# Kernel tuning notes

Measured on AMD Instinct MI355X. Metric: run time of the kernel, lower is better.

## Reference

```python
import jax, jax.numpy as jnp
import numpy as np

N_NODES = 50000
N_EDGES = 600000
DIM = 128
N_LAYERS = 3
N_GRAPHS = 512
BN_EPS = 1e-5


def setup_inputs() -> dict:
    key = jax.random.key(0)
    ks = jax.random.split(key, 8)
    x = jax.random.normal(ks[0], (N_NODES, DIM), dtype=jnp.float32)
    edge_index = jax.random.randint(ks[1], (2, N_EDGES), 0, N_NODES, dtype=jnp.int32)
    batch = jnp.sort(jax.random.randint(ks[2], (N_NODES,), 0, N_GRAPHS, dtype=jnp.int32))
    W1s = jax.random.normal(ks[3], (N_LAYERS, DIM, DIM), dtype=jnp.float32) * (1.0 / np.sqrt(DIM))
    b1s = jnp.zeros((N_LAYERS, DIM), dtype=jnp.float32)
    W2s = jax.random.normal(ks[4], (N_LAYERS, DIM, DIM), dtype=jnp.float32) * (1.0 / np.sqrt(DIM))
    b2s = jnp.zeros((N_LAYERS, DIM), dtype=jnp.float32)
    gammas = jnp.ones((N_LAYERS, DIM), dtype=jnp.float32)
    betas = jnp.zeros((N_LAYERS, DIM), dtype=jnp.float32)
    return {"x": x, "edge_index": edge_index, "batch": batch,
            "W1s": W1s, "b1s": b1s, "W2s": W2s, "b2s": b2s,
            "gammas": gammas, "betas": betas}


def reference(x, edge_index, batch, W1s, b1s, W2s, b2s, gammas, betas):
    # EncoderGIN.forward: stack of GINConv (eps=0) -> ReLU -> BatchNorm1d (train mode),
    # then global_add_pool per layer and concat along feature dim.
    n_nodes = x.shape[0]
    src, dst = edge_index[0], edge_index[1]
    h = x
    pools = []
    for i in range(N_LAYERS):
        # GINConv: aggregate sum of neighbor feats at dst, add (1+0)*self
        agg = jax.ops.segment_sum(h[src], dst, num_segments=n_nodes) + h
        # MLP: Linear -> ReLU -> Linear
        h1 = jax.nn.relu(agg @ W1s[i] + b1s[i])
        h2 = h1 @ W2s[i] + b2s[i]
        # outer ReLU
        h2 = jax.nn.relu(h2)
        # BatchNorm1d, training mode (biased variance over the node dim)
        mean = jnp.mean(h2, axis=0)
        var = jnp.var(h2, axis=0)
        h = (h2 - mean) * jax.lax.rsqrt(var + BN_EPS) * gammas[i] + betas[i]
        pools.append(jax.ops.segment_sum(h, batch, num_segments=N_GRAPHS))
    return jnp.concatenate(pools, axis=1)  # [N_GRAPHS, N_LAYERS*DIM]
```

## Files before the change

### kernel.cpp

```cpp
#include <hip/hip_runtime.h>

#define N_NODES 50000
#define N_EDGES 600000
#define DIM 128
#define N_GRAPHS 512
#define N_LAYERS 3
#define OUT_STRIDE (N_LAYERS * DIM)
#define BN_EPS 1e-5f
#define N_REP 16
#define CAP 64

#define NPB 128
#define NBIN 391
#define BCAP_BIN 3072
#define PADC 16
#define EPB 4096
#define NB3 147

typedef __attribute__((ext_vector_type(8))) short short8;
typedef __attribute__((ext_vector_type(4))) float floatx4;

__device__ inline short f2bf(float f) {
    union { float f; unsigned u; } x{f};
    unsigned r = x.u + 0x7fffu + ((x.u >> 16) & 1u);
    return (short)(r >> 16);
}
__device__ inline float bf2f(short h) {
    union { unsigned u; float f; } x;
    x.u = ((unsigned)(unsigned short)h) << 16;
    return x.f;
}
__device__ inline void split_trunc(float f, short& hi, short& lo) {
    union { float f; unsigned u; } x{f};
    hi = (short)(x.u >> 16);
    union { unsigned u; float f; } hf;
    hf.u = x.u & 0xffff0000u;
    union { float f; unsigned u; } y{f - hf.f};
    lo = (short)(y.u >> 16);
}
__device__ inline floatx4 bf4_to_f4(uint2 w) {
    union { unsigned u; float f; } a, b, c, d;
    a.u = w.x << 16;
    b.u = w.x & 0xffff0000u;
    c.u = w.y << 16;
    d.u = w.y & 0xffff0000u;
    return floatx4{a.f, b.f, c.f, d.f};
}

__global__ __launch_bounds__(256) void prep_scatter_kernel(const int* __restrict__ src,
                                                           const int* __restrict__ dst,
                                                           int* __restrict__ binCur,
                                                           int2* __restrict__ binned,
                                                           const float* __restrict__ W1s,
                                                           const float* __restrict__ W2s,
                                                           short* __restrict__ Whi,
                                                           short* __restrict__ Wlo,
                                                           const float* __restrict__ x,
                                                           short* __restrict__ xb,
                                                           short* __restrict__ hbA,
                                                           short* __restrict__ hbB) {
    if (blockIdx.x < NB3) {
        __shared__ int hist[NBIN];
        __shared__ int basev[NBIN];
        const int t = threadIdx.x;
        for (int b = t; b < NBIN; b += 256) hist[b] = 0;
        __syncthreads();
        const int e0 = blockIdx.x * EPB;
        int sreg[16], dreg[16], rreg[16];
#pragma unroll
        for (int k = 0; k < 16; ++k) {
            int e = e0 + k * 256 + t;
            if (e < N_EDGES) {
                sreg[k] = src[e];
                dreg[k] = dst[e];
            } else {
                dreg[k] = -1;
            }
        }
#pragma unroll
        for (int k = 0; k < 16; ++k)
            if (dreg[k] >= 0) rreg[k] = atomicAdd(&hist[dreg[k] >> 7], 1);
        __syncthreads();
        for (int b = t; b < NBIN; b += 256) {
            int c = hist[b];
            basev[b] = (c > 0) ? atomicAdd(&binCur[b * PADC], c) : 0;
        }
        __syncthreads();
#pragma unroll
        for (int k = 0; k < 16; ++k)
            if (dreg[k] >= 0) {
                int b = dreg[k] >> 7;
                int pos = basev[b] + rreg[k];
                if (pos < BCAP_BIN)
                    binned[(size_t)b * BCAP_BIN + pos] = make_int2(sreg[k], dreg[k] & (NPB - 1));
            }
        return;
    }
    int i = (blockIdx.x - NB3) * 256 + threadIdx.x;
    if (i < 6 * DIM * DIM) {
        int mat = i >> 14;
        int e = i & 16383;
        int k = e >> 7, n = e & 127;
        const float* W = (mat < 3) ? (W1s + (size_t)mat * DIM * DIM)
                                   : (W2s + (size_t)(mat - 3) * DIM * DIM);
        float w = W[e];
        short hi = f2bf(w);
        short lo = f2bf(w - bf2f(hi));
        size_t o = ((size_t)mat << 14) + n * DIM + k;
        Whi[o] = hi;
        Wlo[o] = lo;
    }
    if (i < N_NODES * 32) {
        float4 v = ((const float4*)x)[i];
        unsigned lo = (unsigned short)f2bf(v.x) | ((unsigned)(unsigned short)f2bf(v.y) << 16);
        unsigned hi = (unsigned short)f2bf(v.z) | ((unsigned)(unsigned short)f2bf(v.w) << 16);
        ((uint2*)xb)[i] = make_uint2(lo, hi);
    } else if (i < (N_NODES + 1) * 32) {
        ((uint2*)xb)[i] = make_uint2(0u, 0u);
        ((uint2*)hbA)[i] = make_uint2(0u, 0u);
        ((uint2*)hbB)[i] = make_uint2(0u, 0u);
    }
}

__global__ __launch_bounds__(256) void bucket_build_kernel(const int* __restrict__ binCur,
                                                           const int2* __restrict__ binned,
                                                           int* __restrict__ deg,
                                                           int* __restrict__ esrc) {
    __shared__ int ldeg[NPB];
    __shared__ int lbuck[NPB * CAP];
    const int b = blockIdx.x;
    const int t = threadIdx.x;
    for (int i = t; i < NPB * CAP; i += 256) lbuck[i] = N_NODES;
    if (t < NPB) ldeg[t] = 0;
    __syncthreads();
    int n = binCur[b * PADC];
    if (n > BCAP_BIN) n = BCAP_BIN;
    const int2* bp = binned + (size_t)b * BCAP_BIN;
    for (int i = t; i < n; i += 256) {
        int2 e = bp[i];
        int slot = atomicAdd(&ldeg[e.y], 1);
        if (slot < CAP) lbuck[(e.y << 6) + slot] = e.x;
    }
    __syncthreads();
    const int node0 = b * NPB;
    const int nvalid = min(NPB, N_NODES - node0);
    if (t < NPB && t < nvalid) deg[node0 + t] = ldeg[t];
    const int nu4 = nvalid << 4;
    uint4* d4 = (uint4*)(esrc + ((size_t)node0 << 6));
    const uint4* s4 = (const uint4*)lbuck;
    for (int i = t; i < nu4; i += 256) d4[i] = s4[i];
}

__global__ __launch_bounds__(256, 4) void fused_layer_kernel(
    const short* __restrict__ hin,
    const int* __restrict__ deg,
    const int* __restrict__ esrc,
    const float* __restrict__ prevrep,
    const float* __restrict__ pgamma,
    const float* __restrict__ pbeta,
    const short* __restrict__ W1hi, const short* __restrict__ W1lo,
    const float* __restrict__ b1,
    const short* __restrict__ W2hi, const short* __restrict__ W2lo,
    const float* __restrict__ b2,
    const int* __restrict__ batch,
    short* __restrict__ out,
    float* __restrict__ srep,
    float* __restrict__ gout,
    int layer) {
    __shared__ unsigned sbuf[4096];
    __shared__ float GO_s[256];
    short* As_hi = (short*)sbuf;
    short* As_lo = (short*)(sbuf + 2048);
    const int tid = threadIdx.x;
    const int base = blockIdx.x * 32;

    const int hw = tid >> 5;
    const int l32 = tid & 31;
    int dgr_r[4];
    uint4 idx_r[4][4];
#pragma unroll
    for (int i = 0; i < 4; ++i) {
        int node = base + hw * 4 + i;
        int nc = (node < N_NODES) ? node : (N_NODES - 1);
        dgr_r[i] = deg[nc];
        const uint4* ep = (const uint4*)(esrc + ((size_t)nc << 6));
#pragma unroll
        for (int q = 0; q < 4; ++q) idx_r[i][q] = ep[q];
    }

    if (prevrep) {
        float s = 0.f;
#pragma unroll
        for (int r = 0; r < N_REP; ++r) s += prevrep[r * 256 + tid];
        GO_s[tid] = s;
        __syncthreads();
        if (tid < 128) {
            const float invn = 1.0f / (float)N_NODES;
            float m = GO_s[tid] * invn;
            float var = GO_s[128 + tid] * invn - m * m;
            float G = pgamma[tid] * rsqrtf(var + BN_EPS);
            GO_s[tid] = G;
            GO_s[128 + tid] = pbeta[tid] - m * G;
        }
    } else {
        GO_s[tid] = (tid < 128) ? 1.f : 0.f;
    }
    __syncthreads();

    {
        floatx4 G4 = *(const floatx4*)&GO_s[4 * l32];
        floatx4 O4 = *(const floatx4*)&GO_s[128 + 4 * l32];
        const uint2* hb = (const uint2*)hin;
#pragma unroll
        for (int i = 0; i < 4; ++i) {
            int r = hw * 4 + i;
            int node = base + r;
            floatx4 acc = {0.f, 0.f, 0.f, 0.f};
            if (node < N_NODES) {
                int dgr = dgr_r[i];
                if (dgr > CAP) dgr = CAP;
                uint2 wv[16];
                uint2 wself = hb[(size_t)node * 32 + l32];
#pragma unroll
                for (int q = 0; q < 4; ++q) {
                    uint4 iq = idx_r[i][q];
                    wv[4 * q + 0] = hb[(size_t)iq.x * 32 + l32];
                    wv[4 * q + 1] = hb[(size_t)iq.y * 32 + l32];
                    wv[4 * q + 2] = hb[(size_t)iq.z * 32 + l32];
                    wv[4 * q + 3] = hb[(size_t)iq.w * 32 + l32];
                }
                floatx4 t0 = (bf4_to_f4(wv[0]) + bf4_to_f4(wv[1])) + (bf4_to_f4(wv[2]) + bf4_to_f4(wv[3]));
                floatx4 t1 = (bf4_to_f4(wv[4]) + bf4_to_f4(wv[5])) + (bf4_to_f4(wv[6]) + bf4_to_f4(wv[7]));
                floatx4 t2 = (bf4_to_f4(wv[8]) + bf4_to_f4(wv[9])) + (bf4_to_f4(wv[10]) + bf4_to_f4(wv[11]));
                floatx4 t3 = (bf4_to_f4(wv[12]) + bf4_to_f4(wv[13])) + (bf4_to_f4(wv[14]) + bf4_to_f4(wv[15]));
                acc = bf4_to_f4(wself) + ((t0 + t1) + (t2 + t3));
                if (dgr > 16) {
                    int b0 = node << 6;
                    int jend = b0 + ((dgr + 7) & ~7);
                    for (int j = b0 + 16; j < jend; j += 8) {
                        uint4 i0 = *(const uint4*)&esrc[j];
                        uint4 i1 = *(const uint4*)&esrc[j + 4];
                        uint2 w0 = hb[(size_t)i0.x * 32 + l32];
                        uint2 w1 = hb[(size_t)i0.y * 32 + l32];
                        uint2 w2 = hb[(size_t)i0.z * 32 + l32];
                        uint2 w3 = hb[(size_t)i0.w * 32 + l32];
                        uint2 w4 = hb[(size_t)i1.x * 32 + l32];
                        uint2 w5 = hb[(size_t)i1.y * 32 + l32];
                        uint2 w6 = hb[(size_t)i1.z * 32 + l32];
                        uint2 w7 = hb[(size_t)i1.w * 32 + l32];
                        acc += ((bf4_to_f4(w0) + bf4_to_f4(w1)) + (bf4_to_f4(w2) + bf4_to_f4(w3))) +
                               ((bf4_to_f4(w4) + bf4_to_f4(w5)) + (bf4_to_f4(w6) + bf4_to_f4(w7)));
                    }
                }
                float dp1 = (float)(dgr + 1);
                acc = G4 * acc + dp1 * O4;
            }
            short hi[4], lo[4];
#pragma unroll
            for (int q = 0; q < 4; ++q) split_trunc(acc[q], hi[q], lo[q]);
            unsigned h0 = (unsigned short)hi[0] | ((unsigned)(unsigned short)hi[1] << 16);
            unsigned h1 = (unsigned short)hi[2] | ((unsigned)(unsigned short)hi[3] << 16);
            unsigned l0 = (unsigned short)lo[0] | ((unsigned)(unsigned short)lo[1] << 16);
            unsigned l1 = (unsigned short)lo[2] | ((unsigned)(unsigned short)lo[3] << 16);
            int ch = l32 >> 1, half = l32 & 1;
            int pos = r * 128 + ((ch ^ (r & 15)) * 8) + half * 4;
            *(uint2*)&As_hi[pos] = make_uint2(h0, h1);
            *(uint2*)&As_lo[pos] = make_uint2(l0, l1);
        }
    }
    __syncthreads();

    const int wave = tid >> 6;
    const int lane = tid & 63;
    const int l15 = lane & 15;
    const int quad = lane >> 4;

    floatx4 acc[2][2];
#pragma unroll
    for (int mi = 0; mi < 2; ++mi)
#pragma unroll
        for (int nl = 0; nl < 2; ++nl) acc[mi][nl] = floatx4{0.f, 0.f, 0.f, 0.f};
#pragma unroll
    for (int ks = 0; ks < 4; ++ks) {
        short8 ahi[2], alo[2], bhi[2], blo[2];
#pragma unroll
        for (int mi = 0; mi < 2; ++mi) {
            int row = mi * 16 + l15;
            int pos = row * 128 + (((ks * 4 + quad) ^ l15) * 8);
            ahi[mi] = *(const short8*)&As_hi[pos];
            alo[mi] = *(const short8*)&As_lo[pos];
        }
#pragma unroll
        for (int nl = 0; nl < 2; ++nl) {
            size_t p = (size_t)((wave * 2 + nl) * 16 + l15) * DIM + ks * 32 + quad * 8;
            bhi[nl] = *(const short8*)&W1hi[p];
            blo[nl] = *(const short8*)&W1lo[p];
        }
#pragma unroll
        for (int mi = 0; mi < 2; ++mi)
#pragma unroll
            for (int nl = 0; nl < 2; ++nl) {
                acc[mi][nl] = __builtin_amdgcn_mfma_f32_16x16x32_bf16(ahi[mi], bhi[nl], acc[mi][nl], 0, 0, 0);
                acc[mi][nl] = __builtin_amdgcn_mfma_f32_16x16x32_bf16(alo[mi], bhi[nl], acc[mi][nl], 0, 0, 0);
                acc[mi][nl] = __builtin_amdgcn_mfma_f32_16x16x32_bf16(ahi[mi], blo[nl], acc[mi][nl], 0, 0, 0);
            }
    }
    __syncthreads();

#pragma unroll
    for (int mi = 0; mi < 2; ++mi)
#pragma unroll
        for (int nl = 0; nl < 2; ++nl) {
            int col = (wave * 2 + nl) * 16 + l15;
            float bv = b1[col];
#pragma unroll
            for (int reg = 0; reg < 4; ++reg) {
                int row = mi * 16 + quad * 4 + reg;
                float v = fmaxf(acc[mi][nl][reg] + bv, 0.f);
                union { float f; unsigned u; } x{v};
                union { unsigned u; float f; } hf;
                hf.u = x.u & 0xffff0000u;
                union { float f; unsigned u; } y{v - hf.f};
                unsigned w = hf.u | (y.u >> 16);
                sbuf[row * 128 + ((((col >> 2) ^ (row & 31)) * 4) + (col & 3))] = w;
            }
        }
    __syncthreads();

    floatx4 acc2[2][2];
#pragma unroll
    for (int mi = 0; mi < 2; ++mi)
#pragma unroll
        for (int nl = 0; nl < 2; ++nl) acc2[mi][nl] = floatx4{0.f, 0.f, 0.f, 0.f};
#pragma unroll
    for (int ks = 0; ks < 4; ++ks) {
        short8 ahi2[2], alo2[2], bhi[2], blo[2];
#pragma unroll
        for (int mi = 0; mi < 2; ++mi) {
            int row = mi * 16 + l15;
            int c5 = ks * 8 + quad * 2;
            unsigned w[8];
            *(uint4*)&w[0] = *(const uint4*)&sbuf[row * 128 + ((c5 ^ (row & 31)) * 4)];
            *(uint4*)&w[4] = *(const uint4*)&sbuf[row * 128 + (((c5 + 1) ^ (row & 31)) * 4)];
#pragma unroll
            for (int j = 0; j < 8; ++j) {
                ahi2[mi][j] = (short)(w[j] >> 16);
                alo2[mi][j] = (short)(w[j] & 0xffffu);
            }
        }
#pragma unroll
        for (int nl = 0; nl < 2; ++nl) {
            size_t p = (size_t)((wave * 2 + nl) * 16 + l15) * DIM + ks * 32 + quad * 8;
            bhi[nl] = *(const short8*)&W2hi[p];
            blo[nl] = *(const short8*)&W2lo[p];
        }
#pragma unroll
        for (int mi = 0; mi < 2; ++mi)
#pragma unroll
            for (int nl = 0; nl < 2; ++nl) {
                acc2[mi][nl] = __builtin_amdgcn_mfma_f32_16x16x32_bf16(ahi2[mi], bhi[nl], acc2[mi][nl], 0, 0, 0);
                acc2[mi][nl] = __builtin_amdgcn_mfma_f32_16x16x32_bf16(alo2[mi], bhi[nl], acc2[mi][nl], 0, 0, 0);
                acc2[mi][nl] = __builtin_amdgcn_mfma_f32_16x16x32_bf16(ahi2[mi], blo[nl], acc2[mi][nl], 0, 0, 0);
            }
    }
    __syncthreads();

    float* pool_s = (float*)sbuf;
    float* ssum = (float*)sbuf + 384;
    float* ssq = (float*)sbuf + 512;

    const int g0 = batch[base];
    int idxr[2][4];
#pragma unroll
    for (int mi = 0; mi < 2; ++mi)
#pragma unroll
        for (int reg = 0; reg < 4; ++reg) {
            int row = base + mi * 16 + quad * 4 + reg;
            idxr[mi][reg] = (row < N_NODES) ? (batch[row] - g0) : -1;
        }

#pragma unroll
    for (int nl = 0; nl < 2; ++nl) {
        int col = (wave * 2 + nl) * 16 + l15;
        float bv = b2[col];
        float s_p = 0.f, q_p = 0.f, p0 = 0.f, p1 = 0.f, p2 = 0.f;
#pragma unroll
        for (int mi = 0; mi < 2; ++mi)
#pragma unroll
            for (int reg = 0; reg < 4; ++reg) {
                int idx = idxr[mi][reg];
                if (idx >= 0) {
                    int row = base + mi * 16 + quad * 4 + reg;
                    float v = fmaxf(acc2[mi][nl][reg] + bv, 0.f);
                    out[(size_t)row * DIM + col] = f2bf(v);
                    s_p += v;
                    q_p += v * v;
                    if (idx == 0) p0 += v;
                    else if (idx == 1) p1 += v;
                    else if (idx == 2) p2 += v;
                    else atomicAdd(&gout[(size_t)(g0 + idx) * OUT_STRIDE + layer * DIM + col], v);
                }
            }
        s_p += __shfl_xor(s_p, 16);
        s_p += __shfl_xor(s_p, 32);
        q_p += __shfl_xor(q_p, 16);
        q_p += __shfl_xor(q_p, 32);
        p0 += __shfl_xor(p0, 16);
        p0 += __shfl_xor(p0, 32);
        p1 += __shfl_xor(p1, 16);
        p1 += __shfl_xor(p1, 32);
        p2 += __shfl_xor(p2, 16);
        p2 += __shfl_xor(p2, 32);
        if (quad == 0) {
            ssum[col] = s_p;
            ssq[col] = q_p;
            pool_s[col] = p0;
            pool_s[128 + col] = p1;
            pool_s[256 + col] = p2;
        }
    }
    __syncthreads();

    float* srep_b = srep + (blockIdx.x & (N_REP - 1)) * 256;
    if (tid < 128)
        atomicAdd(&srep_b[tid], ssum[tid]);
    else
        atomicAdd(&srep_b[tid], ssq[tid - 128]);
    for (int i = tid; i < 384; i += 256) {
        int slot = i >> 7, col = i & 127;
        float pv = pool_s[slot * 128 + col];
        int g = g0 + slot;
        if (pv != 0.f && g < N_GRAPHS)
            atomicAdd(&gout[(size_t)g * OUT_STRIDE + layer * DIM + col], pv);
    }
}

__global__ __launch_bounds__(384) void finalize_kernel(const float* __restrict__ rep,
                                                       const float* __restrict__ gammas,
                                                       const float* __restrict__ betas,
                                                       const int* __restrict__ batch,
                                                       float* __restrict__ out) {
    __shared__ float cntf;
    int b = blockIdx.x;
    int t = threadIdx.x;
    if (t == 0) {
        int lo = 0, hi = N_NODES;
        while (lo < hi) {
            int m = (lo + hi) >> 1;
            if (batch[m] < b) lo = m + 1;
            else hi = m;
        }
        int lo2 = lo, hi2 = N_NODES;
        while (lo2 < hi2) {
            int m = (lo2 + hi2) >> 1;
            if (batch[m] < b + 1) lo2 = m + 1;
            else hi2 = m;
        }
        cntf = (float)(lo2 - lo);
    }
    __syncthreads();
    int l = t >> 7, c = t & 127;
    const float* rl = rep + (size_t)l * N_REP * 256;
    float s = 0.f, q = 0.f;
#pragma unroll
    for (int r = 0; r < N_REP; ++r) {
        s += rl[r * 256 + c];
        q += rl[r * 256 + 128 + c];
    }
    const float invn = 1.0f / (float)N_NODES;
    float m = s * invn;
    float var = q * invn - m * m;
    float G = gammas[l * DIM + c] * rsqrtf(var + BN_EPS);
    float OFF = betas[l * DIM + c] - m * G;
    size_t o = (size_t)b * OUT_STRIDE + t;
    out[o] = fmaf(G, out[o], cntf * OFF);
}

extern "C" void kernel_launch(void* const* d_in, const int* in_sizes, int n_in,
                              void* d_out, int out_size, void* d_ws, size_t ws_size,
                              hipStream_t stream) {
    const float* x = (const float*)d_in[0];
    const int* ei = (const int*)d_in[1];
    const int* srcp = ei;
    const int* dstp = ei + N_EDGES;
    const int* batch = (const int*)d_in[2];
    const float* W1s = (const float*)d_in[3];
    const float* b1s = (const float*)d_in[4];
    const float* W2s = (const float*)d_in[5];
    const float* b2s = (const float*)d_in[6];
    const float* gammas = (const float*)d_in[7];
    const float* betas = (const float*)d_in[8];
    float* out = (float*)d_out;

    const size_t NFR = (size_t)(N_NODES + 1) * DIM;
    short* hbufA = (short*)d_ws;
    short* hbufB = hbufA + NFR;
    short* xb = hbufB + NFR;
    short* whi = xb + NFR;
    short* wlo = whi + 6 * DIM * DIM;
    float* stats_rep = (float*)(wlo + 6 * DIM * DIM);
    int* binCur = (int*)(stats_rep + 3 * N_REP * 256);
    int* deg = binCur + NBIN * PADC;
    int* esrc = deg + N_NODES;
    int2* binned = (int2*)hbufB;

    hipMemsetAsync(out, 0, (size_t)N_GRAPHS * OUT_STRIDE * sizeof(float), stream);
    hipMemsetAsync(stats_rep, 0,
                   (3 * N_REP * 256) * sizeof(float) + (NBIN * PADC) * sizeof(int), stream);

    prep_scatter_kernel<<<NB3 + ((N_NODES + 1) * 32 + 255) / 256, 256, 0, stream>>>(
        srcp, dstp, binCur, binned, W1s, W2s, whi, wlo, x, xb, hbufA, hbufB);
    bucket_build_kernel<<<NBIN, 256, 0, stream>>>(binCur, binned, deg, esrc);

    const int nblk = (N_NODES + 31) / 32;
    const short* hin = xb;
    short* hout = hbufA;
    for (int layer = 0; layer < N_LAYERS; ++layer) {
        const float* prevrep =
            (layer == 0) ? nullptr : (stats_rep + (size_t)(layer - 1) * N_REP * 256);
        fused_layer_kernel<<<nblk, 256, 0, stream>>>(
            hin, deg, esrc, prevrep, gammas + (layer - 1) * DIM, betas + (layer - 1) * DIM,
            whi + ((size_t)layer << 14), wlo + ((size_t)layer << 14), b1s + layer * DIM,
            whi + ((size_t)(3 + layer) << 14), wlo + ((size_t)(3 + layer) << 14),
            b2s + layer * DIM, batch, hout, stats_rep + (size_t)layer * N_REP * 256, out, layer);
        hin = hout;
        hout = (hout == hbufA) ? hbufB : hbufA;
    }
    finalize_kernel<<<N_GRAPHS, 384, 0, stream>>>(stats_rep, gammas, betas, batch, out);
}
```

Measured before the change: 285.2 us.

## Process two node tiles per block and batch neighbor gathers in pairs

The fused layer kernel now loops over two 32-node tiles per block, halving the grid to 782 blocks. The per-block BN-coefficient prologue (summing 16 stat replicas) is amortized over both tiles. Neighbor gathers are issued two nodes at a time behind sched barriers to raise memory-level parallelism, and launch bounds drop to 3 waves per SIMD to give room for the extra registers. The risks are lower occupancy and fewer blocks to spread across the CUs, which can leave some idle and add tail imbalance.

```diff
diff --git a/kernel.cpp b/kernel.cpp
--- a/kernel.cpp
+++ b/kernel.cpp
@@ -16,6 +16,10 @@
 #define PADC 16
 #define EPB 4096
 #define NB3 147
+
+#define NTILES 1563
+#define TPB 2
+#define NBLK 782
 
 typedef __attribute__((ext_vector_type(8))) short short8;
 typedef __attribute__((ext_vector_type(4))) float floatx4;
@@ -151,7 +155,7 @@
     for (int i = t; i < nu4; i += 256) d4[i] = s4[i];
 }
 
-__global__ __launch_bounds__(256, 4) void fused_layer_kernel(
+__global__ __launch_bounds__(256, 3) void fused_layer_kernel(
     const short* __restrict__ hin,
     const int* __restrict__ deg,
     const int* __restrict__ esrc,
@@ -172,21 +176,12 @@
     short* As_hi = (short*)sbuf;
     short* As_lo = (short*)(sbuf + 2048);
     const int tid = threadIdx.x;
-    const int base = blockIdx.x * 32;
-
     const int hw = tid >> 5;
     const int l32 = tid & 31;
-    int dgr_r[4];
-    uint4 idx_r[4][4];
-#pragma unroll
-    for (int i = 0; i < 4; ++i) {
-        int node = base + hw * 4 + i;
-        int nc = (node < N_NODES) ? node : (N_NODES - 1);
-        dgr_r[i] = deg[nc];
-        const uint4* ep = (const uint4*)(esrc + ((size_t)nc << 6));
-#pragma unroll
-        for (int q = 0; q < 4; ++q) idx_r[i][q] = ep[q];
-    }
+    const int wave = tid >> 6;
+    const int lane = tid & 63;
+    const int l15 = lane & 15;
+    const int quad = lane >> 4;
 
     if (prevrep) {
         float s = 0.f;
@@ -207,231 +202,264 @@
     }
     __syncthreads();
 
-    {
-        floatx4 G4 = *(const floatx4*)&GO_s[4 * l32];
-        floatx4 O4 = *(const floatx4*)&GO_s[128 + 4 * l32];
-        const uint2* hb = (const uint2*)hin;
-#pragma unroll
-        for (int i = 0; i < 4; ++i) {
-            int r = hw * 4 + i;
-            int node = base + r;
-            floatx4 acc = {0.f, 0.f, 0.f, 0.f};
-            if (node < N_NODES) {
-                int dgr = dgr_r[i];
-                if (dgr > CAP) dgr = CAP;
-                uint2 wv[16];
-                uint2 wself = hb[(size_t)node * 32 + l32];
-#pragma unroll
-                for (int q = 0; q < 4; ++q) {
-                    uint4 iq = idx_r[i][q];
-                    wv[4 * q + 0] = hb[(size_t)iq.x * 32 + l32];
-                    wv[4 * q + 1] = hb[(size_t)iq.y * 32 + l32];
-                    wv[4 * q + 2] = hb[(size_t)iq.z * 32 + l32];
-                    wv[4 * q + 3] = hb[(size_t)iq.w * 32 + l32];
-                }
-                floatx4 t0 = (bf4_to_f4(wv[0]) + bf4_to_f4(wv[1])) + (bf4_to_f4(wv[2]) + bf4_to_f4(wv[3]));
-                floatx4 t1 = (bf4_to_f4(wv[4]) + bf4_to_f4(wv[5])) + (bf4_to_f4(wv[6]) + bf4_to_f4(wv[7]));
-                floatx4 t2 = (bf4_to_f4(wv[8]) + bf4_to_f4(wv[9])) + (bf4_to_f4(wv[10]) + bf4_to_f4(wv[11]));
-                floatx4 t3 = (bf4_to_f4(wv[12]) + bf4_to_f4(wv[13])) + (bf4_to_f4(wv[14]) + bf4_to_f4(wv[15]));
-                acc = bf4_to_f4(wself) + ((t0 + t1) + (t2 + t3));
-                if (dgr > 16) {
-                    int b0 = node << 6;
-                    int jend = b0 + ((dgr + 7) & ~7);
-                    for (int j = b0 + 16; j < jend; j += 8) {
-                        uint4 i0 = *(const uint4*)&esrc[j];
-                        uint4 i1 = *(const uint4*)&esrc[j + 4];
-                        uint2 w0 = hb[(size_t)i0.x * 32 + l32];
-                        uint2 w1 = hb[(size_t)i0.y * 32 + l32];
-                        uint2 w2 = hb[(size_t)i0.z * 32 + l32];
-                        uint2 w3 = hb[(size_t)i0.w * 32 + l32];
-                        uint2 w4 = hb[(size_t)i1.x * 32 + l32];
-                        uint2 w5 = hb[(size_t)i1.y * 32 + l32];
-                        uint2 w6 = hb[(size_t)i1.z * 32 + l32];
-                        uint2 w7 = hb[(size_t)i1.w * 32 + l32];
-                        acc += ((bf4_to_f4(w0) + bf4_to_f4(w1)) + (bf4_to_f4(w2) + bf4_to_f4(w3))) +
-                               ((bf4_to_f4(w4) + bf4_to_f4(w5)) + (bf4_to_f4(w6) + bf4_to_f4(w7)));
+    const uint2* hb = (const uint2*)hin;
+    floatx4 G4 = *(const floatx4*)&GO_s[4 * l32];
+    floatx4 O4 = *(const floatx4*)&GO_s[128 + 4 * l32];
+
+    for (int tk = 0; tk < TPB; ++tk) {
+        const int tile = blockIdx.x * TPB + tk;
+        if (tile >= NTILES) break;
+        const int base = tile * 32;
+
+        {
+            int dgr_r[4];
+            uint4 idx_r[4][4];
+#pragma unroll
+            for (int i = 0; i < 4; ++i) {
+                int node = base + hw * 4 + i;
+                int nc = (node < N_NODES) ? node : (N_NODES - 1);
+                dgr_r[i] = deg[nc];
+                const uint4* ep = (const uint4*)(esrc + ((size_t)nc << 6));
+#pragma unroll
+                for (int q = 0; q < 4; ++q) idx_r[i][q] = ep[q];
+            }
+            __builtin_amdgcn_sched_barrier(0);
+
+#pragma unroll
+            for (int pr = 0; pr < 2; ++pr) {
+                uint2 wself[2];
+                uint2 wv[2][16];
+#pragma unroll
+                for (int ii = 0; ii < 2; ++ii) {
+                    int i = pr * 2 + ii;
+                    int node = base + hw * 4 + i;
+                    int nc = (node < N_NODES) ? node : (N_NODES - 1);
+                    wself[ii] = hb[(size_t)nc * 32 + l32];
+#pragma unroll
+                    for (int q = 0; q < 4; ++q) {
+                        uint4 iq = idx_r[i][q];
+                        wv[ii][4 * q + 0] = hb[(size_t)iq.x * 32 + l32];
+                        wv[ii][4 * q + 1] = hb[(size_t)iq.y * 32 + l32];
+                        wv[ii][4 * q + 2] = hb[(size_t)iq.z * 32 + l32];
+                        wv[ii][4 * q + 3] = hb[(size_t)iq.w * 32 + l32];
                     }
                 }
-                float dp1 = (float)(dgr + 1);
-                acc = G4 * acc + dp1 * O4;
-            }
-            short hi[4], lo[4];
-#pragma unroll
-            for (int q = 0; q < 4; ++q) split_trunc(acc[q], hi[q], lo[q]);
-            unsigned h0 = (unsigned short)hi[0] | ((unsigned)(unsigned short)hi[1] << 16);
-            unsigned h1 = (unsigned short)hi[2] | ((unsigned)(unsigned short)hi[3] << 16);
-            unsigned l0 = (unsigned short)lo[0] | ((unsigned)(unsigned short)lo[1] << 16);
-            unsigned l1 = (unsigned short)lo[2] | ((unsigned)(unsigned short)lo[3] << 16);
-            int ch = l32 >> 1, half = l32 & 1;
-            int pos = r * 128 + ((ch ^ (r & 15)) * 8) + half * 4;
-            *(uint2*)&As_hi[pos] = make_uint2(h0, h1);
-            *(uint2*)&As_lo[pos] = make_uint2(l0, l1);
-        }
-    }
-    __syncthreads();
-
-    const int wave = tid >> 6;
-    const int lane = tid & 63;
-    const int l15 = lane & 15;
-    const int quad = lane >> 4;
-
-    floatx4 acc[2][2];
-#pragma unroll
-    for (int mi = 0; mi < 2; ++mi)
-#pragma unroll
-        for (int nl = 0; nl < 2; ++nl) acc[mi][nl] = floatx4{0.f, 0.f, 0.f, 0.f};
-#pragma unroll
-    for (int ks = 0; ks < 4; ++ks) {
-        short8 ahi[2], alo[2], bhi[2], blo[2];
-#pragma unroll
-        for (int mi = 0; mi < 2; ++mi) {
-            int row = mi * 16 + l15;
-            int pos = row * 128 + (((ks * 4 + quad) ^ l15) * 8);
-            ahi[mi] = *(const short8*)&As_hi[pos];
-            alo[mi] = *(const short8*)&As_lo[pos];
-        }
-#pragma unroll
-        for (int nl = 0; nl < 2; ++nl) {
-            size_t p = (size_t)((wave * 2 + nl) * 16 + l15) * DIM + ks * 32 + quad * 8;
-            bhi[nl] = *(const short8*)&W1hi[p];
-            blo[nl] = *(const short8*)&W1lo[p];
-        }
+                __builtin_amdgcn_sched_barrier(0);
+
+#pragma unroll
+                for (int ii = 0; ii < 2; ++ii) {
+                    int i = pr * 2 + ii;
+                    int r = hw * 4 + i;
+                    int node = base + r;
+                    floatx4 acc = {0.f, 0.f, 0.f, 0.f};
+                    if (node < N_NODES) {
+                        int dgr = dgr_r[i];
+                        if (dgr > CAP) dgr = CAP;
+                        floatx4 t0 = (bf4_to_f4(wv[ii][0]) + bf4_to_f4(wv[ii][1])) +
+                                     (bf4_to_f4(wv[ii][2]) + bf4_to_f4(wv[ii][3]));
+                        floatx4 t1 = (bf4_to_f4(wv[ii][4]) + bf4_to_f4(wv[ii][5])) +
+                                     (bf4_to_f4(wv[ii][6]) + bf4_to_f4(wv[ii][7]));
+                        floatx4 t2 = (bf4_to_f4(wv[ii][8]) + bf4_to_f4(wv[ii][9])) +
+                                     (bf4_to_f4(wv[ii][10]) + bf4_to_f4(wv[ii][11]));
+                        floatx4 t3 = (bf4_to_f4(wv[ii][12]) + bf4_to_f4(wv[ii][13])) +
+                                     (bf4_to_f4(wv[ii][14]) + bf4_to_f4(wv[ii][15]));
+                        acc = bf4_to_f4(wself[ii]) + ((t0 + t1) + (t2 + t3));
+                        if (dgr > 16) {
+                            int b0 = node << 6;
+                            int jend = b0 + ((dgr + 7) & ~7);
+                            for (int j = b0 + 16; j < jend; j += 8) {
+                                uint4 i0 = *(const uint4*)&esrc[j];
+                                uint4 i1 = *(const uint4*)&esrc[j + 4];
+                                uint2 w0 = hb[(size_t)i0.x * 32 + l32];
+                                uint2 w1 = hb[(size_t)i0.y * 32 + l32];
+                                uint2 w2 = hb[(size_t)i0.z * 32 + l32];
+                                uint2 w3 = hb[(size_t)i0.w * 32 + l32];
+                                uint2 w4 = hb[(size_t)i1.x * 32 + l32];
+                                uint2 w5 = hb[(size_t)i1.y * 32 + l32];
+                                uint2 w6 = hb[(size_t)i1.z * 32 + l32];
+                                uint2 w7 = hb[(size_t)i1.w * 32 + l32];
+                                acc += ((bf4_to_f4(w0) + bf4_to_f4(w1)) + (bf4_to_f4(w2) + bf4_to_f4(w3))) +
+                                       ((bf4_to_f4(w4) + bf4_to_f4(w5)) + (bf4_to_f4(w6) + bf4_to_f4(w7)));
+                            }
+                        }
+                        float dp1 = (float)(dgr + 1);
+                        acc = G4 * acc + dp1 * O4;
+                    }
+                    short hi[4], lo[4];
+#pragma unroll
+                    for (int q = 0; q < 4; ++q) split_trunc(acc[q], hi[q], lo[q]);
+                    unsigned h0 = (unsigned short)hi[0] | ((unsigned)(unsigned short)hi[1] << 16);
+                    unsigned h1 = (unsigned short)hi[2] | ((unsigned)(unsigned short)hi[3] << 16);
+                    unsigned l0 = (unsigned short)lo[0] | ((unsigned)(unsigned short)lo[1] << 16);
+                    unsigned l1 = (unsigned short)lo[2] | ((unsigned)(unsigned short)lo[3] << 16);
+                    int ch = l32 >> 1, half = l32 & 1;
+                    int pos = r * 128 + ((ch ^ (r & 15)) * 8) + half * 4;
+                    *(uint2*)&As_hi[pos] = make_uint2(h0, h1);
+                    *(uint2*)&As_lo[pos] = make_uint2(l0, l1);
+                }
+            }
+        }
+        __syncthreads();
+
+        floatx4 acc[2][2];
 #pragma unroll
         for (int mi = 0; mi < 2; ++mi)
 #pragma unroll
+            for (int nl = 0; nl < 2; ++nl) acc[mi][nl] = floatx4{0.f, 0.f, 0.f, 0.f};
+#pragma unroll
+        for (int ks = 0; ks < 4; ++ks) {
+            short8 ahi[2], alo[2], bhi[2], blo[2];
+#pragma unroll
+            for (int mi = 0; mi < 2; ++mi) {
+                int row = mi * 16 + l15;
+                int pos = row * 128 + (((ks * 4 + quad) ^ l15) * 8);
+                ahi[mi] = *(const short8*)&As_hi[pos];
+                alo[mi] = *(const short8*)&As_lo[pos];
+            }
+#pragma unroll
             for (int nl = 0; nl < 2; ++nl) {
-                acc[mi][nl] = __builtin_amdgcn_mfma_f32_16x16x32_bf16(ahi[mi], bhi[nl], acc[mi][nl], 0, 0, 0);
-                acc[mi][nl] = __builtin_amdgcn_mfma_f32_16x16x32_bf16(alo[mi], bhi[nl], acc[mi][nl], 0, 0, 0);
-                acc[mi][nl] = __builtin_amdgcn_mfma_f32_16x16x32_bf16(ahi[mi], blo[nl], acc[mi][nl], 0, 0, 0);
-            }
-    }
-    __syncthreads();
-
-#pragma unroll
-    for (int mi = 0; mi < 2; ++mi)
+                size_t p = (size_t)((wave * 2 + nl) * 16 + l15) * DIM + ks * 32 + quad * 8;
+                bhi[nl] = *(const short8*)&W1hi[p];
+                blo[nl] = *(const short8*)&W1lo[p];
+            }
+#pragma unroll
+            for (int mi = 0; mi < 2; ++mi)
+#pragma unroll
+                for (int nl = 0; nl < 2; ++nl) {
+                    acc[mi][nl] = __builtin_amdgcn_mfma_f32_16x16x32_bf16(ahi[mi], bhi[nl], acc[mi][nl], 0, 0, 0);
+                    acc[mi][nl] = __builtin_amdgcn_mfma_f32_16x16x32_bf16(alo[mi], bhi[nl], acc[mi][nl], 0, 0, 0);
+                    acc[mi][nl] = __builtin_amdgcn_mfma_f32_16x16x32_bf16(ahi[mi], blo[nl], acc[mi][nl], 0, 0, 0);
+                }
+        }
+        __syncthreads();
+
+#pragma unroll
+        for (int mi = 0; mi < 2; ++mi)
+#pragma unroll
+            for (int nl = 0; nl < 2; ++nl) {
+                int col = (wave * 2 + nl) * 16 + l15;
+                float bv = b1[col];
+#pragma unroll
+                for (int reg = 0; reg < 4; ++reg) {
+                    int row = mi * 16 + quad * 4 + reg;
+                    float v = fmaxf(acc[mi][nl][reg] + bv, 0.f);
+                    union { float f; unsigned u; } x{v};
+                    union { unsigned u; float f; } hf;
+                    hf.u = x.u & 0xffff0000u;
+                    union { float f; unsigned u; } y{v - hf.f};
+                    unsigned w = hf.u | (y.u >> 16);
+                    sbuf[row * 128 + ((((col >> 2) ^ (row & 31)) * 4) + (col & 3))] = w;
+                }
+            }
+        __syncthreads();
+
+        floatx4 acc2[2][2];
+#pragma unroll
+        for (int mi = 0; mi < 2; ++mi)
+#pragma unroll
+            for (int nl = 0; nl < 2; ++nl) acc2[mi][nl] = floatx4{0.f, 0.f, 0.f, 0.f};
+#pragma unroll
+        for (int ks = 0; ks < 4; ++ks) {
+            short8 ahi2[2], alo2[2], bhi[2], blo[2];
+#pragma unroll
+            for (int mi = 0; mi < 2; ++mi) {
+                int row = mi * 16 + l15;
+                int c5 = ks * 8 + quad * 2;
+                unsigned w[8];
+                *(uint4*)&w[0] = *(const uint4*)&sbuf[row * 128 + ((c5 ^ (row & 31)) * 4)];
+                *(uint4*)&w[4] = *(const uint4*)&sbuf[row * 128 + (((c5 + 1) ^ (row & 31)) * 4)];
+#pragma unroll
+                for (int j = 0; j < 8; ++j) {
+                    ahi2[mi][j] = (short)(w[j] >> 16);
+                    alo2[mi][j] = (short)(w[j] & 0xffffu);
+                }
+            }
+#pragma unroll
+            for (int nl = 0; nl < 2; ++nl) {
+                size_t p = (size_t)((wave * 2 + nl) * 16 + l15) * DIM + ks * 32 + quad * 8;
+                bhi[nl] = *(const short8*)&W2hi[p];
+                blo[nl] = *(const short8*)&W2lo[p];
+            }
+#pragma unroll
+            for (int mi = 0; mi < 2; ++mi)
+#pragma unroll
+                for (int nl = 0; nl < 2; ++nl) {
+                    acc2[mi][nl] = __builtin_amdgcn_mfma_f32_16x16x32_bf16(ahi2[mi], bhi[nl], acc2[mi][nl], 0, 0, 0);
+                    acc2[mi][nl] = __builtin_amdgcn_mfma_f32_16x16x32_bf16(alo2[mi], bhi[nl], acc2[mi][nl], 0, 0, 0);
+                    acc2[mi][nl] = __builtin_amdgcn_mfma_f32_16x16x32_bf16(ahi2[mi], blo[nl], acc2[mi][nl], 0, 0, 0);
+                }
+        }
+        __syncthreads();
+
+        float* pool_s = (float*)sbuf;
+        float* ssum = (float*)sbuf + 384;
+        float* ssq = (float*)sbuf + 512;
+
+        const int g0 = batch[base];
+        int idxr[2][4];
+#pragma unroll
+        for (int mi = 0; mi < 2; ++mi)
+#pragma unroll
+            for (int reg = 0; reg < 4; ++reg) {
+                int row = base + mi * 16 + quad * 4 + reg;
+                idxr[mi][reg] = (row < N_NODES) ? (batch[row] - g0) : -1;
+            }
+
 #pragma unroll
         for (int nl = 0; nl < 2; ++nl) {
             int col = (wave * 2 + nl) * 16 + l15;
-            float bv = b1[col];
-#pragma unroll
-            for (int reg = 0; reg < 4; ++reg) {
-                int row = mi * 16 + quad * 4 + reg;
-                float v = fmaxf(acc[mi][nl][reg] + bv, 0.f);
-                union { float f; unsigned u; } x{v};
-                union { unsigned u; float f; } hf;
-                hf.u = x.u & 0xffff0000u;
-                union { float f; unsigned u; } y{v - hf.f};
-                unsigned w = hf.u | (y.u >> 16);
-                sbuf[row * 128 + ((((col >> 2) ^ (row & 31)) * 4) + (col & 3))] = w;
-            }
-        }
-    __syncthreads();
-
-    floatx4 acc2[2][2];
-#pragma unroll
-    for (int mi = 0; mi < 2; ++mi)
-#pragma unroll
-        for (int nl = 0; nl < 2; ++nl) acc2[mi][nl] = floatx4{0.f, 0.f, 0.f, 0.f};
-#pragma unroll
-    for (int ks = 0; ks < 4; ++ks) {
-        short8 ahi2[2], alo2[2], bhi[2], blo[2];
-#pragma unroll
-        for (int mi = 0; mi < 2; ++mi) {
-            int row = mi * 16 + l15;
-            int c5 = ks * 8 + quad * 2;
-            unsigned w[8];
-            *(uint4*)&w[0] = *(const uint4*)&sbuf[row * 128 + ((c5 ^ (row & 31)) * 4)];
-            *(uint4*)&w[4] = *(const uint4*)&sbuf[row * 128 + (((c5 + 1) ^ (row & 31)) * 4)];
-#pragma unroll
-            for (int j = 0; j < 8; ++j) {
-                ahi2[mi][j] = (short)(w[j] >> 16);
-                alo2[mi][j] = (short)(w[j] & 0xffffu);
-            }
-        }
-#pragma unroll
-        for (int nl = 0; nl < 2; ++nl) {
-            size_t p = (size_t)((wave * 2 + nl) * 16 + l15) * DIM + ks * 32 + quad * 8;
-            bhi[nl] = *(const short8*)&W2hi[p];
-            blo[nl] = *(const short8*)&W2lo[p];
-        }
-#pragma unroll
-        for (int mi = 0; mi < 2; ++mi)
-#pragma unroll
-            for (int nl = 0; nl < 2; ++nl) {
-                acc2[mi][nl] = __builtin_amdgcn_mfma_f32_16x16x32_bf16(ahi2[mi], bhi[nl], acc2[mi][nl], 0, 0, 0);
-                acc2[mi][nl] = __builtin_amdgcn_mfma_f32_16x16x32_bf16(alo2[mi], bhi[nl], acc2[mi][nl], 0, 0, 0);
-                acc2[mi][nl] = __builtin_amdgcn_mfma_f32_16x16x32_bf16(ahi2[mi], blo[nl], acc2[mi][nl], 0, 0, 0);
-            }
-    }
-    __syncthreads();
-
-    float* pool_s = (float*)sbuf;
-    float* ssum = (float*)sbuf + 384;
-    float* ssq = (float*)sbuf + 512;
-
-    const int g0 = batch[base];
-    int idxr[2][4];
-#pragma unroll
-    for (int mi = 0; mi < 2; ++mi)
-#pragma unroll
-        for (int reg = 0; reg < 4; ++reg) {
-            int row = base + mi * 16 + quad * 4 + reg;
-            idxr[mi][reg] = (row < N_NODES) ? (batch[row] - g0) : -1;
-        }
-
-#pragma unroll
-    for (int nl = 0; nl < 2; ++nl) {
-        int col = (wave * 2 + nl) * 16 + l15;
-        float bv = b2[col];
-        float s_p = 0.f, q_p = 0.f, p0 = 0.f, p1 = 0.f, p2 = 0.f;
-#pragma unroll
-        for (int mi = 0; mi < 2; ++mi)
-#pragma unroll
-            for (int reg = 0; reg < 4; ++reg) {
-                int idx = idxr[mi][reg];
-                if (idx >= 0) {
-                    int row = base + mi * 16 + quad * 4 + reg;
-                    float v = fmaxf(acc2[mi][nl][reg] + bv, 0.f);
-                    out[(size_t)row * DIM + col] = f2bf(v);
-                    s_p += v;
-                    q_p += v * v;
-                    if (idx == 0) p0 += v;
-                    else if (idx == 1) p1 += v;
-                    else if (idx == 2) p2 += v;
-                    else atomicAdd(&gout[(size_t)(g0 + idx) * OUT_STRIDE + layer * DIM + col], v);
-                }
-            }
-        s_p += __shfl_xor(s_p, 16);
-        s_p += __shfl_xor(s_p, 32);
-        q_p += __shfl_xor(q_p, 16);
-        q_p += __shfl_xor(q_p, 32);
-        p0 += __shfl_xor(p0, 16);
-        p0 += __shfl_xor(p0, 32);
-        p1 += __shfl_xor(p1, 16);
-        p1 += __shfl_xor(p1, 32);
-        p2 += __shfl_xor(p2, 16);
-        p2 += __shfl_xor(p2, 32);
-        if (quad == 0) {
-            ssum[col] = s_p;
-            ssq[col] = q_p;
-            pool_s[col] = p0;
-            pool_s[128 + col] = p1;
-            pool_s[256 + col] = p2;
-        }
-    }
-    __syncthreads();
-
-    float* srep_b = srep + (blockIdx.x & (N_REP - 1)) * 256;
-    if (tid < 128)
-        atomicAdd(&srep_b[tid], ssum[tid]);
-    else
-        atomicAdd(&srep_b[tid], ssq[tid - 128]);
-    for (int i = tid; i < 384; i += 256) {
-        int slot = i >> 7, col = i & 127;
-        float pv = pool_s[slot * 128 + col];
-        int g = g0 + slot;
-        if (pv != 0.f && g < N_GRAPHS)
-            atomicAdd(&gout[(size_t)g * OUT_STRIDE + layer * DIM + col], pv);
+            float bv = b2[col];
+            float s_p = 0.f, q_p = 0.f, p0 = 0.f, p1 = 0.f, p2 = 0.f;
+#pragma unroll
+            for (int mi = 0; mi < 2; ++mi)
+#pragma unroll
+                for (int reg = 0; reg < 4; ++reg) {
+                    int idx = idxr[mi][reg];
+                    if (idx >= 0) {
+                        int row = base + mi * 16 + quad * 4 + reg;
+                        float v = fmaxf(acc2[mi][nl][reg] + bv, 0.f);
+                        out[(size_t)row * DIM + col] = f2bf(v);
+                        s_p += v;
+                        q_p += v * v;
+                        if (idx == 0) p0 += v;
+                        else if (idx == 1) p1 += v;
+                        else if (idx == 2) p2 += v;
+                        else atomicAdd(&gout[(size_t)(g0 + idx) * OUT_STRIDE + layer * DIM + col], v);
+                    }
+                }
+            s_p += __shfl_xor(s_p, 16);
+            s_p += __shfl_xor(s_p, 32);
+            q_p += __shfl_xor(q_p, 16);
+            q_p += __shfl_xor(q_p, 32);
+            p0 += __shfl_xor(p0, 16);
+            p0 += __shfl_xor(p0, 32);
+            p1 += __shfl_xor(p1, 16);
+            p1 += __shfl_xor(p1, 32);
+            p2 += __shfl_xor(p2, 16);
+            p2 += __shfl_xor(p2, 32);
+            if (quad == 0) {
+                ssum[col] = s_p;
+                ssq[col] = q_p;
+                pool_s[col] = p0;
+                pool_s[128 + col] = p1;
+                pool_s[256 + col] = p2;
+            }
+        }
+        __syncthreads();
+
+        float* srep_b = srep + (blockIdx.x & (N_REP - 1)) * 256;
+        if (tid < 128)
+            atomicAdd(&srep_b[tid], ssum[tid]);
+        else
+            atomicAdd(&srep_b[tid], ssq[tid - 128]);
+        for (int i = tid; i < 384; i += 256) {
+            int slot = i >> 7, col = i & 127;
+            float pv = pool_s[slot * 128 + col];
+            int g = g0 + slot;
+            if (pv != 0.f && g < N_GRAPHS)
+                atomicAdd(&gout[(size_t)g * OUT_STRIDE + layer * DIM + col], pv);
+        }
+        if (tk + 1 < TPB) __syncthreads();
     }
 }
 
@@ -512,13 +540,12 @@
         srcp, dstp, binCur, binned, W1s, W2s, whi, wlo, x, xb, hbufA, hbufB);
     bucket_build_kernel<<<NBIN, 256, 0, stream>>>(binCur, binned, deg, esrc);
 
-    const int nblk = (N_NODES + 31) / 32;
     const short* hin = xb;
     short* hout = hbufA;
     for (int layer = 0; layer < N_LAYERS; ++layer) {
         const float* prevrep =
             (layer == 0) ? nullptr : (stats_rep + (size_t)(layer - 1) * N_REP * 256);
-        fused_layer_kernel<<<nblk, 256, 0, stream>>>(
+        fused_layer_kernel<<<NBLK, 256, 0, stream>>>(
             hin, deg, esrc, prevrep, gammas + (layer - 1) * DIM, betas + (layer - 1) * DIM,
             whi + ((size_t)layer << 14), wlo + ((size_t)layer << 14), b1s + layer * DIM,
             whi + ((size_t)(3 + layer) << 14), wlo + ((size_t)(3 + layer) << 14),
```

New measurement: 434.8 us. 52.5% more time.

## Split fused layer into separate gather-aggregate and MLP kernels via global buffer

Applied to the files above, without the earlier changes.

Splits the per-layer fused kernel into an aggregation kernel and an MLP kernel. The aggregation kernel walks nodes with a grid-stride loop and writes packed hi/lo bf16 split values for each node to a global buffer. The MLP kernel loads 32-row tiles from that buffer into swizzled shared memory and unpacks the hi/lo halves before the MFMAs. The aim is to let the latency-bound gather run at its own occupancy, separate from the MFMA work, with a higher occupancy hint on the MLP kernel. In exchange it adds an extra round trip of a 50k×128×4-byte buffer through global memory and one more launch per layer.

```diff
diff --git a/kernel.cpp b/kernel.cpp
--- a/kernel.cpp
+++ b/kernel.cpp
@@ -16,6 +16,10 @@
 #define PADC 16
 #define EPB 4096
 #define NB3 147
+
+#define NTILES 1563
+#define NPAD (NTILES * 32)
+#define AGG_BLOCKS 2048
 
 typedef __attribute__((ext_vector_type(8))) short short8;
 typedef __attribute__((ext_vector_type(4))) float floatx4;
@@ -151,13 +155,104 @@
     for (int i = t; i < nu4; i += 256) d4[i] = s4[i];
 }
 
-__global__ __launch_bounds__(256, 4) void fused_layer_kernel(
-    const short* __restrict__ hin,
-    const int* __restrict__ deg,
-    const int* __restrict__ esrc,
-    const float* __restrict__ prevrep,
-    const float* __restrict__ pgamma,
-    const float* __restrict__ pbeta,
+__global__ __launch_bounds__(256) void agg_kernel(const short* __restrict__ hin,
+                                                  const int* __restrict__ deg,
+                                                  const int* __restrict__ esrc,
+                                                  const float* __restrict__ prevrep,
+                                                  const float* __restrict__ pgamma,
+                                                  const float* __restrict__ pbeta,
+                                                  unsigned* __restrict__ agg) {
+    __shared__ float GO_s[256];
+    const int tid = threadIdx.x;
+    if (prevrep) {
+        float s = 0.f;
+#pragma unroll
+        for (int r = 0; r < N_REP; ++r) s += prevrep[r * 256 + tid];
+        GO_s[tid] = s;
+        __syncthreads();
+        if (tid < 128) {
+            const float invn = 1.0f / (float)N_NODES;
+            float m = GO_s[tid] * invn;
+            float var = GO_s[128 + tid] * invn - m * m;
+            float G = pgamma[tid] * rsqrtf(var + BN_EPS);
+            GO_s[tid] = G;
+            GO_s[128 + tid] = pbeta[tid] - m * G;
+        }
+    } else {
+        GO_s[tid] = (tid < 128) ? 1.f : 0.f;
+    }
+    __syncthreads();
+
+    const int hw = tid >> 5;
+    const int l32 = tid & 31;
+    floatx4 G4 = *(const floatx4*)&GO_s[4 * l32];
+    floatx4 O4 = *(const floatx4*)&GO_s[128 + 4 * l32];
+    const uint2* hb = (const uint2*)hin;
+
+    for (int node = blockIdx.x * 8 + hw; node < NPAD; node += AGG_BLOCKS * 8) {
+        floatx4 acc = {0.f, 0.f, 0.f, 0.f};
+        if (node < N_NODES) {
+            int dgr = deg[node];
+            if (dgr > CAP) dgr = CAP;
+            const uint4* ep = (const uint4*)(esrc + ((size_t)node << 6));
+            uint4 q0 = ep[0], q1 = ep[1], q2 = ep[2], q3 = ep[3];
+            uint2 wself = hb[(size_t)node * 32 + l32];
+            uint2 wv[16];
+            wv[0] = hb[(size_t)q0.x * 32 + l32];
+            wv[1] = hb[(size_t)q0.y * 32 + l32];
+            wv[2] = hb[(size_t)q0.z * 32 + l32];
+            wv[3] = hb[(size_t)q0.w * 32 + l32];
+            wv[4] = hb[(size_t)q1.x * 32 + l32];
+            wv[5] = hb[(size_t)q1.y * 32 + l32];
+            wv[6] = hb[(size_t)q1.z * 32 + l32];
+            wv[7] = hb[(size_t)q1.w * 32 + l32];
+            wv[8] = hb[(size_t)q2.x * 32 + l32];
+            wv[9] = hb[(size_t)q2.y * 32 + l32];
+            wv[10] = hb[(size_t)q2.z * 32 + l32];
+            wv[11] = hb[(size_t)q2.w * 32 + l32];
+            wv[12] = hb[(size_t)q3.x * 32 + l32];
+            wv[13] = hb[(size_t)q3.y * 32 + l32];
+            wv[14] = hb[(size_t)q3.z * 32 + l32];
+            wv[15] = hb[(size_t)q3.w * 32 + l32];
+            floatx4 t0 = (bf4_to_f4(wv[0]) + bf4_to_f4(wv[1])) + (bf4_to_f4(wv[2]) + bf4_to_f4(wv[3]));
+            floatx4 t1 = (bf4_to_f4(wv[4]) + bf4_to_f4(wv[5])) + (bf4_to_f4(wv[6]) + bf4_to_f4(wv[7]));
+            floatx4 t2 = (bf4_to_f4(wv[8]) + bf4_to_f4(wv[9])) + (bf4_to_f4(wv[10]) + bf4_to_f4(wv[11]));
+            floatx4 t3 = (bf4_to_f4(wv[12]) + bf4_to_f4(wv[13])) + (bf4_to_f4(wv[14]) + bf4_to_f4(wv[15]));
+            acc = bf4_to_f4(wself) + ((t0 + t1) + (t2 + t3));
+            if (dgr > 16) {
+                int b0 = node << 6;
+                int jend = b0 + ((dgr + 7) & ~7);
+                for (int j = b0 + 16; j < jend; j += 8) {
+                    uint4 i0 = *(const uint4*)&esrc[j];
+                    uint4 i1 = *(const uint4*)&esrc[j + 4];
+                    uint2 w0 = hb[(size_t)i0.x * 32 + l32];
+                    uint2 w1 = hb[(size_t)i0.y * 32 + l32];
+                    uint2 w2 = hb[(size_t)i0.z * 32 + l32];
+                    uint2 w3 = hb[(size_t)i0.w * 32 + l32];
+                    uint2 w4 = hb[(size_t)i1.x * 32 + l32];
+                    uint2 w5 = hb[(size_t)i1.y * 32 + l32];
+                    uint2 w6 = hb[(size_t)i1.z * 32 + l32];
+                    uint2 w7 = hb[(size_t)i1.w * 32 + l32];
+                    acc += ((bf4_to_f4(w0) + bf4_to_f4(w1)) + (bf4_to_f4(w2) + bf4_to_f4(w3))) +
+                           ((bf4_to_f4(w4) + bf4_to_f4(w5)) + (bf4_to_f4(w6) + bf4_to_f4(w7)));
+                }
+            }
+            float dp1 = (float)(dgr + 1);
+            acc = G4 * acc + dp1 * O4;
+        }
+        short hi[4], lo[4];
+#pragma unroll
+        for (int q = 0; q < 4; ++q) split_trunc(acc[q], hi[q], lo[q]);
+        unsigned p0 = ((unsigned)(unsigned short)hi[0] << 16) | (unsigned short)lo[0];
+        unsigned p1 = ((unsigned)(unsigned short)hi[1] << 16) | (unsigned short)lo[1];
+        unsigned p2 = ((unsigned)(unsigned short)hi[2] << 16) | (unsigned short)lo[2];
+        unsigned p3 = ((unsigned)(unsigned short)hi[3] << 16) | (unsigned short)lo[3];
+        *(uint4*)&agg[(size_t)node * 128 + 4 * l32] = make_uint4(p0, p1, p2, p3);
+    }
+}
+
+__global__ __launch_bounds__(256, 6) void mlp_kernel(
+    const unsigned* __restrict__ agg,
     const short* __restrict__ W1hi, const short* __restrict__ W1lo,
     const float* __restrict__ b1,
     const short* __restrict__ W2hi, const short* __restrict__ W2lo,
@@ -168,104 +263,17 @@
     float* __restrict__ gout,
     int layer) {
     __shared__ unsigned sbuf[4096];
-    __shared__ float GO_s[256];
-    short* As_hi = (short*)sbuf;
-    short* As_lo = (short*)(sbuf + 2048);
     const int tid = threadIdx.x;
     const int base = blockIdx.x * 32;
 
-    const int hw = tid >> 5;
-    const int l32 = tid & 31;
-    int dgr_r[4];
-    uint4 idx_r[4][4];
-#pragma unroll
-    for (int i = 0; i < 4; ++i) {
-        int node = base + hw * 4 + i;
-        int nc = (node < N_NODES) ? node : (N_NODES - 1);
-        dgr_r[i] = deg[nc];
-        const uint4* ep = (const uint4*)(esrc + ((size_t)nc << 6));
-#pragma unroll
-        for (int q = 0; q < 4; ++q) idx_r[i][q] = ep[q];
-    }
-
-    if (prevrep) {
-        float s = 0.f;
-#pragma unroll
-        for (int r = 0; r < N_REP; ++r) s += prevrep[r * 256 + tid];
-        GO_s[tid] = s;
-        __syncthreads();
-        if (tid < 128) {
-            const float invn = 1.0f / (float)N_NODES;
-            float m = GO_s[tid] * invn;
-            float var = GO_s[128 + tid] * invn - m * m;
-            float G = pgamma[tid] * rsqrtf(var + BN_EPS);
-            GO_s[tid] = G;
-            GO_s[128 + tid] = pbeta[tid] - m * G;
-        }
-    } else {
-        GO_s[tid] = (tid < 128) ? 1.f : 0.f;
-    }
-    __syncthreads();
-
     {
-        floatx4 G4 = *(const floatx4*)&GO_s[4 * l32];
-        floatx4 O4 = *(const floatx4*)&GO_s[128 + 4 * l32];
-        const uint2* hb = (const uint2*)hin;
-#pragma unroll
-        for (int i = 0; i < 4; ++i) {
-            int r = hw * 4 + i;
-            int node = base + r;
-            floatx4 acc = {0.f, 0.f, 0.f, 0.f};
-            if (node < N_NODES) {
-                int dgr = dgr_r[i];
-                if (dgr > CAP) dgr = CAP;
-                uint2 wv[16];
-                uint2 wself = hb[(size_t)node * 32 + l32];
-#pragma unroll
-                for (int q = 0; q < 4; ++q) {
-                    uint4 iq = idx_r[i][q];
-                    wv[4 * q + 0] = hb[(size_t)iq.x * 32 + l32];
-                    wv[4 * q + 1] = hb[(size_t)iq.y * 32 + l32];
-                    wv[4 * q + 2] = hb[(size_t)iq.z * 32 + l32];
-                    wv[4 * q + 3] = hb[(size_t)iq.w * 32 + l32];
-                }
-                floatx4 t0 = (bf4_to_f4(wv[0]) + bf4_to_f4(wv[1])) + (bf4_to_f4(wv[2]) + bf4_to_f4(wv[3]));
-                floatx4 t1 = (bf4_to_f4(wv[4]) + bf4_to_f4(wv[5])) + (bf4_to_f4(wv[6]) + bf4_to_f4(wv[7]));
-                floatx4 t2 = (bf4_to_f4(wv[8]) + bf4_to_f4(wv[9])) + (bf4_to_f4(wv[10]) + bf4_to_f4(wv[11]));
-                floatx4 t3 = (bf4_to_f4(wv[12]) + bf4_to_f4(wv[13])) + (bf4_to_f4(wv[14]) + bf4_to_f4(wv[15]));
-                acc = bf4_to_f4(wself) + ((t0 + t1) + (t2 + t3));
-                if (dgr > 16) {
-                    int b0 = node << 6;
-                    int jend = b0 + ((dgr + 7) & ~7);
-                    for (int j = b0 + 16; j < jend; j += 8) {
-                        uint4 i0 = *(const uint4*)&esrc[j];
-                        uint4 i1 = *(const uint4*)&esrc[j + 4];
-                        uint2 w0 = hb[(size_t)i0.x * 32 + l32];
-                        uint2 w1 = hb[(size_t)i0.y * 32 + l32];
-                        uint2 w2 = hb[(size_t)i0.z * 32 + l32];
-                        uint2 w3 = hb[(size_t)i0.w * 32 + l32];
-                        uint2 w4 = hb[(size_t)i1.x * 32 + l32];
-                        uint2 w5 = hb[(size_t)i1.y * 32 + l32];
-                        uint2 w6 = hb[(size_t)i1.z * 32 + l32];
-                        uint2 w7 = hb[(size_t)i1.w * 32 + l32];
-                        acc += ((bf4_to_f4(w0) + bf4_to_f4(w1)) + (bf4_to_f4(w2) + bf4_to_f4(w3))) +
-                               ((bf4_to_f4(w4) + bf4_to_f4(w5)) + (bf4_to_f4(w6) + bf4_to_f4(w7)));
-                    }
-                }
-                float dp1 = (float)(dgr + 1);
-                acc = G4 * acc + dp1 * O4;
-            }
-            short hi[4], lo[4];
-#pragma unroll
-            for (int q = 0; q < 4; ++q) split_trunc(acc[q], hi[q], lo[q]);
-            unsigned h0 = (unsigned short)hi[0] | ((unsigned)(unsigned short)hi[1] << 16);
-            unsigned h1 = (unsigned short)hi[2] | ((unsigned)(unsigned short)hi[3] << 16);
-            unsigned l0 = (unsigned short)lo[0] | ((unsigned)(unsigned short)lo[1] << 16);
-            unsigned l1 = (unsigned short)lo[2] | ((unsigned)(unsigned short)lo[3] << 16);
-            int ch = l32 >> 1, half = l32 & 1;
-            int pos = r * 128 + ((ch ^ (r & 15)) * 8) + half * 4;
-            *(uint2*)&As_hi[pos] = make_uint2(h0, h1);
-            *(uint2*)&As_lo[pos] = make_uint2(l0, l1);
+        const uint4* gs = (const uint4*)(agg + (size_t)base * 128);
+#pragma unroll
+        for (int k = 0; k < 4; ++k) {
+            uint4 v = gs[k * 256 + tid];
+            int idx = (k * 256 + tid) * 4;
+            int row = idx >> 7, c0 = idx & 127;
+            *(uint4*)&sbuf[row * 128 + (((c0 >> 2) ^ (row & 31)) << 2)] = v;
         }
     }
     __syncthreads();
@@ -286,9 +294,15 @@
 #pragma unroll
         for (int mi = 0; mi < 2; ++mi) {
             int row = mi * 16 + l15;
-            int pos = row * 128 + (((ks * 4 + quad) ^ l15) * 8);
-            ahi[mi] = *(const short8*)&As_hi[pos];
-            alo[mi] = *(const short8*)&As_lo[pos];
+            int c5 = ks * 8 + quad * 2;
+            unsigned w[8];
+            *(uint4*)&w[0] = *(const uint4*)&sbuf[row * 128 + ((c5 ^ (row & 31)) * 4)];
+            *(uint4*)&w[4] = *(const uint4*)&sbuf[row * 128 + (((c5 + 1) ^ (row & 31)) * 4)];
+#pragma unroll
+            for (int j = 0; j < 8; ++j) {
+                ahi[mi][j] = (short)(w[j] >> 16);
+                alo[mi][j] = (short)(w[j] & 0xffffu);
+            }
         }
 #pragma unroll
         for (int nl = 0; nl < 2; ++nl) {
@@ -502,6 +516,7 @@
     int* binCur = (int*)(stats_rep + 3 * N_REP * 256);
     int* deg = binCur + NBIN * PADC;
     int* esrc = deg + N_NODES;
+    unsigned* agg = (unsigned*)(esrc + (size_t)N_NODES * CAP);
     int2* binned = (int2*)hbufB;
 
     hipMemsetAsync(out, 0, (size_t)N_GRAPHS * OUT_STRIDE * sizeof(float), stream);
@@ -512,15 +527,15 @@
         srcp, dstp, binCur, binned, W1s, W2s, whi, wlo, x, xb, hbufA, hbufB);
     bucket_build_kernel<<<NBIN, 256, 0, stream>>>(binCur, binned, deg, esrc);
 
-    const int nblk = (N_NODES + 31) / 32;
     const short* hin = xb;
     short* hout = hbufA;
     for (int layer = 0; layer < N_LAYERS; ++layer) {
         const float* prevrep =
             (layer == 0) ? nullptr : (stats_rep + (size_t)(layer - 1) * N_REP * 256);
-        fused_layer_kernel<<<nblk, 256, 0, stream>>>(
-            hin, deg, esrc, prevrep, gammas + (layer - 1) * DIM, betas + (layer - 1) * DIM,
-            whi + ((size_t)layer << 14), wlo + ((size_t)layer << 14), b1s + layer * DIM,
+        agg_kernel<<<AGG_BLOCKS, 256, 0, stream>>>(
+            hin, deg, esrc, prevrep, gammas + (layer - 1) * DIM, betas + (layer - 1) * DIM, agg);
+        mlp_kernel<<<NTILES, 256, 0, stream>>>(
+            agg, whi + ((size_t)layer << 14), wlo + ((size_t)layer << 14), b1s + layer * DIM,
             whi + ((size_t)(3 + layer) << 14), wlo + ((size_t)(3 + layer) << 14),
             b2s + layer * DIM, batch, hout, stats_rep + (size_t)layer * N_REP * 256, out, layer);
         hin = hout;
```

Measured after the change: 304.3 us. +6.7%, slower.
